# Performance work log

Measured on AMD Instinct MI355X. Metric: run time of the kernel, lower is better.

Reference implementation:

```python
import jax, jax.numpy as jnp
import numpy as np

B, S, HID = 1, 2048, 4096
NH, KVH, D = 32, 8, 128
MAXP = 2048
EPS = 1e-6


def _rope_tables(max_pos, dim, base=10000.0):
    inv_freq = 1.0 / (base ** (np.arange(0, dim, 2, dtype=np.float32) / dim))
    t = np.arange(max_pos, dtype=np.float32)
    freqs = np.outer(t, inv_freq)                      # [max_pos, dim/2]
    emb = np.concatenate([freqs, freqs], axis=-1)      # [max_pos, dim]
    return jnp.asarray(np.cos(emb)), jnp.asarray(np.sin(emb))


def setup_inputs() -> dict:
    key = jax.random.key(0)
    ks = jax.random.split(key, 6)
    x = jax.random.normal(ks[0], (B, S, HID), jnp.float32)
    scale = 0.02
    wq = jax.random.normal(ks[1], (NH * D, HID), jnp.float32) * scale
    wk = jax.random.normal(ks[2], (KVH * D, HID), jnp.float32) * scale
    wv = jax.random.normal(ks[3], (KVH * D, HID), jnp.float32) * scale
    wo = jax.random.normal(ks[4], (NH * D, HID), jnp.float32).T * scale  # stored as [HID, NH*D] -> transpose back
    wo = jnp.asarray(jax.random.normal(ks[4], (HID, NH * D), jnp.float32) * scale)
    cos_table, sin_table = _rope_tables(MAXP, D)
    return {
        "x": x, "wq": wq, "wk": wk, "wv": wv, "wo": wo,
        "q_norm_w": jnp.ones((D,), jnp.float32),
        "k_norm_w": jnp.ones((D,), jnp.float32),
        "cos_table": cos_table, "sin_table": sin_table,
        "k_cache": jnp.zeros((1, B, MAXP, KVH, D), jnp.float32),
        "v_cache": jnp.zeros((1, B, MAXP, KVH, D), jnp.float32),
        "positions": jnp.arange(S, dtype=jnp.int32),
        "layer_idx": 0,
    }


def _rmsnorm(x, w):
    return w * (x * jax.lax.rsqrt(jnp.mean(x * x, axis=-1, keepdims=True) + EPS))


def _rope(x, cos, sin):
    # x: [B, H, S, D]; cos/sin: [1, 1, S, D]
    half = x.shape[-1] // 2
    x1, x2 = x[..., :half], x[..., half:]
    rotated = jnp.concatenate([-x2, x1], axis=-1)
    return x * cos + rotated * sin


def reference(x, wq, wk, wv, wo, q_norm_w, k_norm_w, cos_table, sin_table,
              k_cache, v_cache, positions, layer_idx):
    bsz, seq_len, _ = x.shape
    d = q_norm_w.shape[0]
    nh = wq.shape[0] // d
    kvh = wk.shape[0] // d
    g = nh // kvh

    q = (x @ wq.T).reshape(bsz, seq_len, nh, d).transpose(0, 2, 1, 3)    # [B,NH,S,D]
    k = (x @ wk.T).reshape(bsz, seq_len, kvh, d).transpose(0, 2, 1, 3)   # [B,KVH,S,D]
    v = (x @ wv.T).reshape(bsz, seq_len, kvh, d).transpose(0, 2, 1, 3)

    q = _rmsnorm(q, q_norm_w)
    k = _rmsnorm(k, k_norm_w)

    cos = cos_table[positions][None, None]  # [1,1,S,D]
    sin = sin_table[positions][None, None]
    q = _rope(q, cos, sin)
    k = _rope(k, cos, sin)

    # KV-cache scatter at dynamic positions (prefill: positions = arange(S))
    kc = k_cache[layer_idx].at[:, positions].set(k.transpose(0, 2, 1, 3))
    vc = v_cache[layer_idx].at[:, positions].set(v.transpose(0, 2, 1, 3))
    # K = max(positions)+1 == seq_len in this (prefill) setup; static for jit
    K = seq_len
    k_all = kc[:, :K].transpose(0, 2, 1, 3)   # [B,KVH,K,D]
    v_all = vc[:, :K].transpose(0, 2, 1, 3)

    # GQA: group query heads instead of repeat_interleave on K/V (same math)
    qg = q.reshape(bsz, kvh, g, seq_len, d)
    scale = 1.0 / jnp.sqrt(jnp.asarray(d, q.dtype))
    scores = jnp.einsum('bkgqd,bkld->bkgql', qg, k_all) * scale
    causal = jnp.tril(jnp.ones((seq_len, K), dtype=bool))
    scores = jnp.where(causal, scores, jnp.finfo(scores.dtype).min)
    attn = jax.nn.softmax(scores, axis=-1)
    out = jnp.einsum('bkgql,bkld->bkgqd', attn, v_all)
    out = out.reshape(bsz, nh, seq_len, d).transpose(0, 2, 1, 3).reshape(bsz, seq_len, nh * d)
    return out @ wo.T
```

## Files before the change

### kernel.cpp

```cpp
#include <hip/hip_runtime.h>

typedef unsigned short u16;
typedef unsigned int u32;
typedef __attribute__((ext_vector_type(8))) short bf16x8;
typedef __attribute__((ext_vector_type(4))) float f32x4;
struct __align__(8) us4 { u16 x, y, z, w; };

#define S_LEN 2048
#define HID   4096
#define NH    32
#define KVH   8
#define HD    128
#define MFMA16 __builtin_amdgcn_mfma_f32_16x16x32_bf16

__device__ inline u16 f2bf(float f) {
  u32 u = __float_as_uint(f);
  u32 r = (u + 0x7fffu + ((u >> 16) & 1u)) >> 16;
  return (u16)r;
}
__device__ inline float bf2f(u16 h) { return __uint_as_float(((u32)h) << 16); }

__device__ inline void gld_lds16(const void* g, void* l) {
  __builtin_amdgcn_global_load_lds(
      (const __attribute__((address_space(1))) u32*)g,
      (__attribute__((address_space(3))) u32*)l, 16, 0, 0);
}

__global__ __launch_bounds__(256)
void cvt_all(const float* __restrict__ x, const float* __restrict__ wq,
             const float* __restrict__ wk, const float* __restrict__ wv,
             const float* __restrict__ wo, u16* __restrict__ xb,
             u16* __restrict__ wqb, u16* __restrict__ wkb,
             u16* __restrict__ wvb, u16* __restrict__ wob) {
  int b = blockIdx.x;
  const float* in; u16* out; int base;
  if (b < 8192)       { in = x;  out = xb;  base = b; }
  else if (b < 24576) { in = wq; out = wqb; base = b - 8192; }
  else if (b < 28672) { in = wk; out = wkb; base = b - 24576; }
  else if (b < 32768) { in = wv; out = wvb; base = b - 28672; }
  else                { in = wo; out = wob; base = b - 32768; }
  size_t i = ((size_t)base * 256 + threadIdx.x) * 4;
  f32x4 v = *(const f32x4*)(in + i);
  us4 o;
  o.x = f2bf(v[0]); o.y = f2bf(v[1]); o.z = f2bf(v[2]); o.w = f2bf(v[3]);
  *(us4*)(out + i) = o;
}

__device__ __forceinline__ void stage_half(const u16* __restrict__ src, int ldk,
                                           int rowBase, int k0, char* lslot,
                                           int t) {
  int rl = t >> 3;
  int c8 = ((t & 7) ^ (rl & 7)) * 8;
  gld_lds16(src + (size_t)(rowBase + rl) * ldk + k0 + c8, lslot + t * 16);
  gld_lds16(src + (size_t)(rowBase + 64 + rl) * ldk + k0 + c8,
            lslot + 8192 + t * 16);
}

__device__ __forceinline__ void gemm256_core(
    const u16* __restrict__ A, const u16* __restrict__ W, int m0, int n0,
    int ldk, int kBeg, int kEnd, char* lds, f32x4 (&acc)[8][4]) {
  const int t = threadIdx.x;
  const int l = t & 63, w = t >> 6;
  const int l15 = l & 15, quad = l >> 4;
  const int wr = w >> 2, wcn = w & 3;
  const int nt = (kEnd - kBeg) >> 6;
  char* ldsA = lds;
  char* ldsB = lds + 65536;
  const int swz0 = ((0 + quad) ^ (l15 & 7)) * 16;
  const int swz1 = ((4 + quad) ^ (l15 & 7)) * 16;
  const int aB0 = wr * 16384 + l15 * 128;
  const int bB0 = wcn * 8192 + l15 * 128;

#pragma unroll
  for (int m = 0; m < 8; m++)
#pragma unroll
    for (int n = 0; n < 4; n++) acc[m][n] = (f32x4){0.f, 0.f, 0.f, 0.f};

  stage_half(W, ldk, n0,       kBeg, ldsB,         t);
  stage_half(A, ldk, m0,       kBeg, ldsA,         t);
  stage_half(W, ldk, n0 + 128, kBeg, ldsB + 16384, t);
  stage_half(A, ldk, m0 + 128, kBeg, ldsA + 16384, t);
  if (nt > 1) {
    stage_half(W, ldk, n0, kBeg + 64, ldsB + 32768, t);
    stage_half(A, ldk, m0, kBeg + 64, ldsA + 32768, t);
    asm volatile("s_waitcnt vmcnt(4)" ::: "memory");
  } else {
    asm volatile("s_waitcnt vmcnt(0)" ::: "memory");
  }
  __builtin_amdgcn_s_barrier();

  bf16x8 a[4][2], b[2][2], b2[2][2];
#pragma unroll 1
  for (int tt = 0; tt < nt; ++tt) {
    const int d = tt & 1, dn = d ^ 1;
    const int aO = d * 32768 + aB0;
    const int bO = d * 32768 + bB0;
    const int k1 = kBeg + (tt + 1) * 64;
    const int k2 = k1 + 64;

#pragma unroll
    for (int m = 0; m < 4; m++) {
      a[m][0] = *(const bf16x8*)(ldsA + aO + m * 2048 + swz0);
      a[m][1] = *(const bf16x8*)(ldsA + aO + m * 2048 + swz1);
    }
#pragma unroll
    for (int n = 0; n < 2; n++) {
      b[n][0] = *(const bf16x8*)(ldsB + bO + n * 2048 + swz0);
      b[n][1] = *(const bf16x8*)(ldsB + bO + n * 2048 + swz1);
    }
    if (tt + 1 < nt) stage_half(W, ldk, n0 + 128, k1, ldsB + dn * 32768 + 16384, t);
    __builtin_amdgcn_s_barrier();
    __builtin_amdgcn_s_setprio(1);
#pragma unroll
    for (int m = 0; m < 4; m++)
#pragma unroll
      for (int n = 0; n < 2; n++) {
        acc[m][n] = MFMA16(a[m][0], b[n][0], acc[m][n], 0, 0, 0);
        acc[m][n] = MFMA16(a[m][1], b[n][1], acc[m][n], 0, 0, 0);
      }
    __builtin_amdgcn_s_setprio(0);
    __builtin_amdgcn_s_barrier();

#pragma unroll
    for (int n = 0; n < 2; n++) {
      b2[n][0] = *(const bf16x8*)(ldsB + bO + (2 + n) * 2048 + swz0);
      b2[n][1] = *(const bf16x8*)(ldsB + bO + (2 + n) * 2048 + swz1);
    }
    if (tt + 1 < nt) stage_half(A, ldk, m0 + 128, k1, ldsA + dn * 32768 + 16384, t);
    __builtin_amdgcn_s_barrier();
    __builtin_amdgcn_s_setprio(1);
#pragma unroll
    for (int m = 0; m < 4; m++)
#pragma unroll
      for (int n = 0; n < 2; n++) {
        acc[m][2 + n] = MFMA16(a[m][0], b2[n][0], acc[m][2 + n], 0, 0, 0);
        acc[m][2 + n] = MFMA16(a[m][1], b2[n][1], acc[m][2 + n], 0, 0, 0);
      }
    __builtin_amdgcn_s_setprio(0);
    __builtin_amdgcn_s_barrier();

#pragma unroll
    for (int m = 0; m < 4; m++) {
      a[m][0] = *(const bf16x8*)(ldsA + aO + (4 + m) * 2048 + swz0);
      a[m][1] = *(const bf16x8*)(ldsA + aO + (4 + m) * 2048 + swz1);
    }
    if (tt + 2 < nt) stage_half(W, ldk, n0, k2, ldsB + d * 32768, t);
    __builtin_amdgcn_s_barrier();
    __builtin_amdgcn_s_setprio(1);
#pragma unroll
    for (int m = 0; m < 4; m++)
#pragma unroll
      for (int n = 0; n < 2; n++) {
        acc[4 + m][n] = MFMA16(a[m][0], b[n][0], acc[4 + m][n], 0, 0, 0);
        acc[4 + m][n] = MFMA16(a[m][1], b[n][1], acc[4 + m][n], 0, 0, 0);
      }
    __builtin_amdgcn_s_setprio(0);
    __builtin_amdgcn_s_barrier();

    if (tt + 2 < nt) stage_half(A, ldk, m0, k2, ldsA + d * 32768, t);
    __builtin_amdgcn_s_barrier();
    __builtin_amdgcn_s_setprio(1);
#pragma unroll
    for (int m = 0; m < 4; m++)
#pragma unroll
      for (int n = 0; n < 2; n++) {
        acc[4 + m][2 + n] = MFMA16(a[m][0], b2[n][0], acc[4 + m][2 + n], 0, 0, 0);
        acc[4 + m][2 + n] = MFMA16(a[m][1], b2[n][1], acc[4 + m][2 + n], 0, 0, 0);
      }
    __builtin_amdgcn_s_setprio(0);
    if (tt + 1 < nt) {
      if (tt + 2 < nt) asm volatile("s_waitcnt vmcnt(4)" ::: "memory");
      else             asm volatile("s_waitcnt vmcnt(0)" ::: "memory");
    }
    __builtin_amdgcn_s_barrier();
  }
}

__global__ __launch_bounds__(512, 2)
void gemm_qkv8(const u16* __restrict__ xb, const u16* __restrict__ wqb,
               const u16* __restrict__ wkb, const u16* __restrict__ wvb,
               u16* __restrict__ Qp, u16* __restrict__ Kp, u16* __restrict__ vt) {
  extern __shared__ char lds[];
  const int id = blockIdx.x;
  const int sw = (id & 7) * 24 + (id >> 3);
  const int bx = sw % 24, by = sw / 24;
  const u16* W; u16* C; int n0, ldc, epi;
  if (bx < 16)      { W = wqb; C = Qp; n0 = bx * 256;        ldc = HID;  epi = 0; }
  else if (bx < 20) { W = wkb; C = Kp; n0 = (bx - 16) * 256; ldc = 1024; epi = 0; }
  else              { W = wvb; C = vt; n0 = (bx - 20) * 256; ldc = 0;    epi = 1; }
  const int m0 = by * 256;

  f32x4 acc[8][4];
  gemm256_core(xb, W, m0, n0, HID, 0, HID, lds, acc);

  const int t = threadIdx.x, l = t & 63, w = t >> 6;
  const int l15 = l & 15, quad = l >> 4;
  const int wr = w >> 2, wcn = w & 3;
  if (epi == 0) {
#pragma unroll
    for (int m = 0; m < 8; m++) {
      int row0 = m0 + wr * 128 + m * 16 + quad * 4;
#pragma unroll
      for (int n = 0; n < 4; n++) {
        int col = n0 + wcn * 64 + n * 16 + l15;
#pragma unroll
        for (int r = 0; r < 4; r++)
          C[(size_t)(row0 + r) * ldc + col] = f2bf(acc[m][n][r]);
      }
    }
  } else {
#pragma unroll
    for (int m = 0; m < 8; m++) {
      int row0 = m0 + wr * 128 + m * 16 + quad * 4;
#pragma unroll
      for (int n = 0; n < 4; n++) {
        int col = n0 + wcn * 64 + n * 16 + l15;
        us4 v;
        v.x = f2bf(acc[m][n][0]); v.y = f2bf(acc[m][n][1]);
        v.z = f2bf(acc[m][n][2]); v.w = f2bf(acc[m][n][3]);
        *(us4*)(vt + (size_t)col * S_LEN + row0) = v;
      }
    }
  }
}

__global__ __launch_bounds__(512, 2)
void gemm_out8(const u16* __restrict__ ab, const u16* __restrict__ wob,
               float* __restrict__ O0, float* __restrict__ O1) {
  extern __shared__ char lds[];
  const int id = blockIdx.x;
  const int sw = (id & 7) * 32 + (id >> 3);
  const int z = sw >> 7, rem = sw & 127;
  const int by = rem >> 4, bx = rem & 15;
  float* Op = z ? O1 : O0;

  f32x4 acc[8][4];
  gemm256_core(ab, wob, by * 256, bx * 256, HID, z * 2048, z * 2048 + 2048, lds, acc);

  const int t = threadIdx.x, l = t & 63, w = t >> 6;
  const int l15 = l & 15, quad = l >> 4;
  const int wr = w >> 2, wcn = w & 3;
#pragma unroll
  for (int m = 0; m < 8; m++) {
    int row0 = by * 256 + wr * 128 + m * 16 + quad * 4;
#pragma unroll
    for (int n = 0; n < 4; n++) {
      int col = bx * 256 + wcn * 64 + n * 16 + l15;
#pragma unroll
      for (int r = 0; r < 4; r++)
        Op[(size_t)(row0 + r) * HID + col] = acc[m][n][r];
    }
  }
}

__global__ __launch_bounds__(256)
void reduce_out(const float* __restrict__ O0, const float* __restrict__ O1,
                float* __restrict__ outp) {
  size_t i = ((size_t)blockIdx.x * 256 + threadIdx.x) * 4;
  f32x4 a = *(const f32x4*)(O0 + i);
  f32x4 b = *(const f32x4*)(O1 + i);
  a[0] += b[0]; a[1] += b[1]; a[2] += b[2]; a[3] += b[3];
  *(f32x4*)(outp + i) = a;
}

__global__ __launch_bounds__(256)
void rope_all(const u16* __restrict__ Qp, const u16* __restrict__ Kp,
              const float* __restrict__ qnw, const float* __restrict__ knw,
              const float* __restrict__ cosT, const float* __restrict__ sinT,
              const int* __restrict__ pos, u16* __restrict__ qbh,
              u16* __restrict__ kbh) {
  const int b = blockIdx.x;
  const int t = threadIdx.x, w = t >> 6, l = t & 63;
  const u16* xr; const float* nw; u16* orow; int s;
  if (b < 16384) {
    int p = b * 4 + w;
    s = p >> 5; int h = p & 31;
    xr = Qp + (size_t)s * HID + h * HD;
    nw = qnw;
    orow = qbh + ((size_t)h * S_LEN + s) * HD;
  } else {
    int p = (b - 16384) * 4 + w;
    s = p >> 3; int h = p & 7;
    xr = Kp + (size_t)s * 1024 + h * HD;
    nw = knw;
    orow = kbh + ((size_t)h * S_LEN + s) * HD;
  }
  float x1 = bf2f(xr[l]);
  float x2 = bf2f(xr[l + 64]);
  float ss = x1 * x1 + x2 * x2;
#pragma unroll
  for (int m = 1; m < 64; m <<= 1) ss += __shfl_xor(ss, m);
  float rinv = rsqrtf(ss * (1.0f / 128.0f) + 1e-6f);
  float n1 = x1 * rinv * nw[l];
  float n2 = x2 * rinv * nw[l + 64];
  int ps = pos[s];
  float c1 = cosT[ps * HD + l], s1 = sinT[ps * HD + l];
  float c2 = cosT[ps * HD + l + 64], s2 = sinT[ps * HD + l + 64];
  float y1 = n1 * c1 - n2 * s1;
  float y2 = n2 * c2 + n1 * s2;
  orow[l] = f2bf(y1);
  orow[l + 64] = f2bf(y2);
}

__global__ __launch_bounds__(256)
void attn_fwd(const u16* __restrict__ qh, const u16* __restrict__ kbh,
              const u16* __restrict__ vth, u16* __restrict__ ab) {
  __shared__ __align__(16) u16 lK[64 * 128];
  __shared__ __align__(16) u16 lV[128 * 64];
  __shared__ __align__(16) u16 lP[4][16 * 72];
  const int t = threadIdx.x, w = t >> 6, l = t & 63;
  const int quad = l >> 4, l15 = l & 15;
  const int h = blockIdx.x;
  const int qt = 31 - blockIdx.y;
  const int kvh = h >> 2;
  const int q0 = qt * 64;
  const int qrow = q0 + w * 16 + l15;

  bf16x8 qf[4];
#pragma unroll
  for (int ks = 0; ks < 4; ks++)
    qf[ks] = *(const bf16x8*)(qh + ((size_t)h * S_LEN + qrow) * HD + ks * 32 + quad * 8);

  f32x4 accO[8];
#pragma unroll
  for (int j = 0; j < 8; j++) accO[j] = (f32x4){0.f, 0.f, 0.f, 0.f};
  float m_cur = -3.0e38f, l_sum = 0.f;
  const float scale = 0.08838834764831845f;

  const int ntiles = qt + 1;
  for (int tt = 0; tt < ntiles; tt++) {
    const int c0 = tt * 64;
#pragma unroll
    for (int i = 0; i < 4; i++) {
      int Cc = i * 256 + t;
      int r = Cc >> 4, ch = Cc & 15;
      int gch = ch ^ (r & 15);
      gld_lds16(kbh + ((size_t)kvh * S_LEN + c0 + r) * HD + gch * 8, lK + Cc * 8);
    }
#pragma unroll
    for (int i = 0; i < 4; i++) {
      int Cc = i * 256 + t;
      int d = Cc >> 3, ch = Cc & 7;
      int gch = ch ^ (d & 7);
      gld_lds16(vth + ((size_t)kvh * HD + d) * S_LEN + c0 + gch * 8, lV + Cc * 8);
    }
    __syncthreads();

    f32x4 st[4];
#pragma unroll
    for (int i = 0; i < 4; i++) {
      f32x4 sa = (f32x4){0.f, 0.f, 0.f, 0.f};
      int r = i * 16 + l15;
#pragma unroll
      for (int ks = 0; ks < 4; ks++) {
        int lc = ks * 4 + quad;
        bf16x8 kf = *(const bf16x8*)(lK + r * 128 + ((lc ^ (r & 15)) * 8));
        sa = __builtin_amdgcn_mfma_f32_16x16x32_bf16(kf, qf[ks], sa, 0, 0, 0);
      }
      st[i] = sa;
    }

    float tmax = -3.0e38f;
#pragma unroll
    for (int i = 0; i < 4; i++) {
#pragma unroll
      for (int r = 0; r < 4; r++) {
        int kcol = c0 + i * 16 + quad * 4 + r;
        float v = st[i][r] * scale;
        v = (kcol <= qrow) ? v : -3.0e38f;
        st[i][r] = v;
        tmax = fmaxf(tmax, v);
      }
    }
    tmax = fmaxf(tmax, __shfl_xor(tmax, 16));
    tmax = fmaxf(tmax, __shfl_xor(tmax, 32));
    float m_new = fmaxf(m_cur, tmax);
    float alpha = __expf(m_cur - m_new);

    float psum = 0.f;
#pragma unroll
    for (int i = 0; i < 4; i++) {
      us4 pv;
      u16* pp = (u16*)&pv;
#pragma unroll
      for (int r = 0; r < 4; r++) {
        float pe = __expf(st[i][r] - m_new);
        psum += pe;
        pp[r] = f2bf(pe);
      }
      *(us4*)(&lP[w][l15 * 72 + i * 16 + quad * 4]) = pv;
    }
    psum += __shfl_xor(psum, 16);
    psum += __shfl_xor(psum, 32);
    l_sum = l_sum * alpha + psum;
    m_cur = m_new;

#pragma unroll
    for (int r = 0; r < 4; r++) {
      float ar = __shfl(alpha, quad * 4 + r);
#pragma unroll
      for (int j = 0; j < 8; j++) accO[j][r] *= ar;
    }

    bf16x8 pf[2];
#pragma unroll
    for (int ks = 0; ks < 2; ks++)
      pf[ks] = *(const bf16x8*)(&lP[w][l15 * 72 + ks * 32 + quad * 8]);
#pragma unroll
    for (int j = 0; j < 8; j++) {
      int d = j * 16 + l15;
#pragma unroll
      for (int ks = 0; ks < 2; ks++) {
        int lc = ks * 4 + quad;
        bf16x8 vf = *(const bf16x8*)(lV + d * 64 + ((lc ^ (d & 7)) * 8));
        accO[j] = __builtin_amdgcn_mfma_f32_16x16x32_bf16(pf[ks], vf, accO[j], 0, 0, 0);
      }
    }
    __syncthreads();
  }

  float linv = 1.0f / l_sum;
#pragma unroll
  for (int r = 0; r < 4; r++) {
    float lr = __shfl(linv, quad * 4 + r);
    int row = q0 + w * 16 + quad * 4 + r;
#pragma unroll
    for (int j = 0; j < 8; j++) {
      int col = h * HD + j * 16 + l15;
      ab[(size_t)row * HID + col] = f2bf(accO[j][r] * lr);
    }
  }
}

extern "C" void kernel_launch(void* const* d_in, const int* in_sizes, int n_in,
                              void* d_out, int out_size, void* d_ws, size_t ws_size,
                              hipStream_t stream) {
  const float* x    = (const float*)d_in[0];
  const float* wq   = (const float*)d_in[1];
  const float* wk   = (const float*)d_in[2];
  const float* wv   = (const float*)d_in[3];
  const float* wo   = (const float*)d_in[4];
  const float* qnw  = (const float*)d_in[5];
  const float* knw  = (const float*)d_in[6];
  const float* cosT = (const float*)d_in[7];
  const float* sinT = (const float*)d_in[8];
  const int* positions = (const int*)d_in[11];

  static int attr_done = 0;
  if (!attr_done) {
    hipFuncSetAttribute((const void*)gemm_qkv8,
                        hipFuncAttributeMaxDynamicSharedMemorySize, 131072);
    hipFuncSetAttribute((const void*)gemm_out8,
                        hipFuncAttributeMaxDynamicSharedMemorySize, 131072);
    attr_done = 1;
  }

  char* ws = (char*)d_ws;
  u16* xb  = (u16*)(ws + 0ULL);
  u16* wqb = (u16*)(ws + 16777216ULL);
  u16* wkb = (u16*)(ws + 50331648ULL);
  u16* wvb = (u16*)(ws + 58720256ULL);
  u16* wob = (u16*)(ws + 67108864ULL);
  u16* Qp  = (u16*)(ws + 100663296ULL);
  u16* Kp  = (u16*)(ws + 117440512ULL);
  u16* vt  = (u16*)(ws + 121634816ULL);
  u16* qbh = (u16*)(ws + 125829120ULL);
  u16* kbh = (u16*)(ws + 142606336ULL);
  u16* ab  = (u16*)(ws + 146800640ULL);
  float* O0 = (float*)(ws + 0ULL);
  float* O1 = (float*)(ws + 33554432ULL);

  cvt_all<<<49152, 256, 0, stream>>>(x, wq, wk, wv, wo, xb, wqb, wkb, wvb, wob);

  gemm_qkv8<<<192, 512, 131072, stream>>>(xb, wqb, wkb, wvb, Qp, Kp, vt);

  rope_all<<<20480, 256, 0, stream>>>(Qp, Kp, qnw, knw, cosT, sinT, positions,
                                      qbh, kbh);

  attn_fwd<<<dim3(NH, S_LEN / 64), 256, 0, stream>>>(qbh, kbh, vt, ab);

  gemm_out8<<<256, 512, 131072, stream>>>(ab, wob, O0, O1);
  reduce_out<<<8192, 256, 0, stream>>>(O0, O1, (float*)d_out);
}
```

Before: 509.5 us.

## Overlap wo conversion with QKV GEMM and restructure K-loop prefetch schedule

New measurement: 492.7 us. 1.03x faster.

```diff
diff --git a/kernel.cpp b/kernel.cpp
--- a/kernel.cpp
+++ b/kernel.cpp
@@ -29,16 +29,14 @@
 __global__ __launch_bounds__(256)
 void cvt_all(const float* __restrict__ x, const float* __restrict__ wq,
              const float* __restrict__ wk, const float* __restrict__ wv,
-             const float* __restrict__ wo, u16* __restrict__ xb,
-             u16* __restrict__ wqb, u16* __restrict__ wkb,
-             u16* __restrict__ wvb, u16* __restrict__ wob) {
+             u16* __restrict__ xb, u16* __restrict__ wqb,
+             u16* __restrict__ wkb, u16* __restrict__ wvb) {
   int b = blockIdx.x;
   const float* in; u16* out; int base;
   if (b < 8192)       { in = x;  out = xb;  base = b; }
   else if (b < 24576) { in = wq; out = wqb; base = b - 8192; }
   else if (b < 28672) { in = wk; out = wkb; base = b - 24576; }
-  else if (b < 32768) { in = wv; out = wvb; base = b - 28672; }
-  else                { in = wo; out = wob; base = b - 32768; }
+  else                { in = wv; out = wvb; base = b - 28672; }
   size_t i = ((size_t)base * 256 + threadIdx.x) * 4;
   f32x4 v = *(const f32x4*)(in + i);
   us4 o;
@@ -77,13 +75,15 @@
     for (int n = 0; n < 4; n++) acc[m][n] = (f32x4){0.f, 0.f, 0.f, 0.f};
 
   stage_half(W, ldk, n0,       kBeg, ldsB,         t);
+  stage_half(W, ldk, n0 + 128, kBeg, ldsB + 16384, t);
   stage_half(A, ldk, m0,       kBeg, ldsA,         t);
-  stage_half(W, ldk, n0 + 128, kBeg, ldsB + 16384, t);
   stage_half(A, ldk, m0 + 128, kBeg, ldsA + 16384, t);
   if (nt > 1) {
-    stage_half(W, ldk, n0, kBeg + 64, ldsB + 32768, t);
-    stage_half(A, ldk, m0, kBeg + 64, ldsA + 32768, t);
-    asm volatile("s_waitcnt vmcnt(4)" ::: "memory");
+    stage_half(W, ldk, n0,       kBeg + 64, ldsB + 32768,         t);
+    stage_half(W, ldk, n0 + 128, kBeg + 64, ldsB + 32768 + 16384, t);
+    stage_half(A, ldk, m0,       kBeg + 64, ldsA + 32768,         t);
+    stage_half(A, ldk, m0 + 128, kBeg + 64, ldsA + 32768 + 16384, t);
+    asm volatile("s_waitcnt vmcnt(8)" ::: "memory");
   } else {
     asm volatile("s_waitcnt vmcnt(0)" ::: "memory");
   }
@@ -92,11 +92,11 @@
   bf16x8 a[4][2], b[2][2], b2[2][2];
 #pragma unroll 1
   for (int tt = 0; tt < nt; ++tt) {
-    const int d = tt & 1, dn = d ^ 1;
+    const int d = tt & 1;
     const int aO = d * 32768 + aB0;
     const int bO = d * 32768 + bB0;
-    const int k1 = kBeg + (tt + 1) * 64;
-    const int k2 = k1 + 64;
+    const int k2 = kBeg + (tt + 2) * 64;
+    const bool pf = (tt + 2 < nt);
 
 #pragma unroll
     for (int m = 0; m < 4; m++) {
@@ -108,7 +108,6 @@
       b[n][0] = *(const bf16x8*)(ldsB + bO + n * 2048 + swz0);
       b[n][1] = *(const bf16x8*)(ldsB + bO + n * 2048 + swz1);
     }
-    if (tt + 1 < nt) stage_half(W, ldk, n0 + 128, k1, ldsB + dn * 32768 + 16384, t);
     __builtin_amdgcn_s_barrier();
     __builtin_amdgcn_s_setprio(1);
 #pragma unroll
@@ -126,7 +125,6 @@
       b2[n][0] = *(const bf16x8*)(ldsB + bO + (2 + n) * 2048 + swz0);
       b2[n][1] = *(const bf16x8*)(ldsB + bO + (2 + n) * 2048 + swz1);
     }
-    if (tt + 1 < nt) stage_half(A, ldk, m0 + 128, k1, ldsA + dn * 32768 + 16384, t);
     __builtin_amdgcn_s_barrier();
     __builtin_amdgcn_s_setprio(1);
 #pragma unroll
@@ -139,12 +137,15 @@
     __builtin_amdgcn_s_setprio(0);
     __builtin_amdgcn_s_barrier();
 
+    if (pf) {
+      stage_half(W, ldk, n0,       k2, ldsB + d * 32768,         t);
+      stage_half(W, ldk, n0 + 128, k2, ldsB + d * 32768 + 16384, t);
+    }
 #pragma unroll
     for (int m = 0; m < 4; m++) {
       a[m][0] = *(const bf16x8*)(ldsA + aO + (4 + m) * 2048 + swz0);
       a[m][1] = *(const bf16x8*)(ldsA + aO + (4 + m) * 2048 + swz1);
     }
-    if (tt + 2 < nt) stage_half(W, ldk, n0, k2, ldsB + d * 32768, t);
     __builtin_amdgcn_s_barrier();
     __builtin_amdgcn_s_setprio(1);
 #pragma unroll
@@ -157,7 +158,10 @@
     __builtin_amdgcn_s_setprio(0);
     __builtin_amdgcn_s_barrier();
 
-    if (tt + 2 < nt) stage_half(A, ldk, m0, k2, ldsA + d * 32768, t);
+    if (pf) {
+      stage_half(A, ldk, m0,       k2, ldsA + d * 32768,         t);
+      stage_half(A, ldk, m0 + 128, k2, ldsA + d * 32768 + 16384, t);
+    }
     __builtin_amdgcn_s_barrier();
     __builtin_amdgcn_s_setprio(1);
 #pragma unroll
@@ -168,10 +172,8 @@
         acc[4 + m][2 + n] = MFMA16(a[m][1], b2[n][1], acc[4 + m][2 + n], 0, 0, 0);
       }
     __builtin_amdgcn_s_setprio(0);
-    if (tt + 1 < nt) {
-      if (tt + 2 < nt) asm volatile("s_waitcnt vmcnt(4)" ::: "memory");
-      else             asm volatile("s_waitcnt vmcnt(0)" ::: "memory");
-    }
+    if (pf) asm volatile("s_waitcnt vmcnt(8)" ::: "memory");
+    else    asm volatile("s_waitcnt vmcnt(0)" ::: "memory");
     __builtin_amdgcn_s_barrier();
   }
 }
@@ -179,9 +181,23 @@
 __global__ __launch_bounds__(512, 2)
 void gemm_qkv8(const u16* __restrict__ xb, const u16* __restrict__ wqb,
                const u16* __restrict__ wkb, const u16* __restrict__ wvb,
-               u16* __restrict__ Qp, u16* __restrict__ Kp, u16* __restrict__ vt) {
+               u16* __restrict__ Qp, u16* __restrict__ Kp, u16* __restrict__ vt,
+               const float* __restrict__ wo, u16* __restrict__ wob) {
   extern __shared__ char lds[];
   const int id = blockIdx.x;
+  if (id >= 192) {
+    int cb = id - 192;
+    size_t base = ((size_t)cb * 512 + threadIdx.x) * 4;
+#pragma unroll 1
+    for (int it = 0; it < 128; ++it) {
+      size_t i = base + (size_t)it * 131072;
+      f32x4 v = *(const f32x4*)(wo + i);
+      us4 o;
+      o.x = f2bf(v[0]); o.y = f2bf(v[1]); o.z = f2bf(v[2]); o.w = f2bf(v[3]);
+      *(us4*)(wob + i) = o;
+    }
+    return;
+  }
   const int sw = (id & 7) * 24 + (id >> 3);
   const int bx = sw % 24, by = sw / 24;
   const u16* W; u16* C; int n0, ldc, epi;
@@ -470,9 +486,9 @@
   float* O0 = (float*)(ws + 0ULL);
   float* O1 = (float*)(ws + 33554432ULL);
 
-  cvt_all<<<49152, 256, 0, stream>>>(x, wq, wk, wv, wo, xb, wqb, wkb, wvb, wob);
-
-  gemm_qkv8<<<192, 512, 131072, stream>>>(xb, wqb, wkb, wvb, Qp, Kp, vt);
+  cvt_all<<<32768, 256, 0, stream>>>(x, wq, wk, wv, xb, wqb, wkb, wvb);
+
+  gemm_qkv8<<<256, 512, 131072, stream>>>(xb, wqb, wkb, wvb, Qp, Kp, vt, wo, wob);
 
   rope_all<<<20480, 256, 0, stream>>>(Qp, Kp, qnw, knw, cosT, sinT, positions,
                                       qbh, kbh);
```
